# Optimization experiments

Hardware: AMD Instinct MI355X
Metric: run time of the kernel (lower is better)

## Reference

```python
import jax, jax.numpy as jnp
import numpy as np

M2 = 512  # config['sketch_dim_AV']; seq_len must be divisible by M2


def setup_inputs() -> dict:
    key = jax.random.key(0)
    kq, kk, kv = jax.random.split(key, 3)
    B, H, N, D = 4, 16, 4096, 64
    Q = jax.random.normal(kq, (B, H, N, D), dtype=jnp.float32)
    K = jax.random.normal(kk, (B, H, N, D), dtype=jnp.float32)
    V = jax.random.normal(kv, (B, H, N, D), dtype=jnp.float32)
    mask = jnp.ones((B, N), dtype=jnp.float32)  # unused: self.mask == False
    return {"Q": Q, "K": K, "V": V, "mask": mask}


def reference(Q, K, V, mask):
    # SketchingAttention.forward with sketch_QT=False, method='averaging',
    # sketch_AV=True, use_relu=False, skip_V=True, mask disabled.
    B, H, N, D = Q.shape
    scale = D ** 0.5
    # right_sketch_3D on KS = K.transpose(-1,-2) (shape b,h,d,n):
    # torch does reshape(b*h, d, n) -> reshape(b, h, m2, n//m2, d).mean(-2).
    # Row-major reshape semantics match jnp.reshape exactly, including the
    # intentional (d,n)->(m2, n//m2, d) block reinterpretation.
    SKS = jnp.swapaxes(K, -1, -2).reshape(B, H, M2, N // M2, D).mean(axis=-2)  # (B,H,M2,D)
    # compute_attn(QS, SKS): softmax(Q @ SKS^T / sqrt(d)) over the sketch axis
    logits = jnp.einsum('bhnd,bhmd->bhnm', Q, SKS) / scale  # (B,H,N,M2)
    A_est = jax.nn.softmax(logits, axis=-1)
    # ST_V: chunk-average V along the sequence into M2 buckets
    ST_V = V.reshape(B, H, M2, N // M2, D).mean(axis=-2)  # (B,H,M2,D)
    AV_est = jnp.einsum('bhnm,bhmd->bhnd', A_est, ST_V)
    return AV_est + V  # skip_V residual
```

## Files before the change

kernel.cpp:

```cpp
#include <hip/hip_runtime.h>

using short8 = __attribute__((ext_vector_type(8))) short;
using f32x4  = __attribute__((ext_vector_type(4))) float;

constexpr int NN = 4096;
constexpr int DD = 64;
constexpr int MM = 512;
constexpr int BH = 64;

__device__ __forceinline__ short f2bf(float f) {
    union { float f; unsigned u; } v; v.f = f;
    unsigned r = v.u + 0x7FFF + ((v.u >> 16) & 1);
    return (short)(r >> 16);
}

__device__ __forceinline__ unsigned cvt_pk_bf16(float lo, float hi) {
    unsigned r;
    asm("v_cvt_pk_bf16_f32 %0, %1, %2" : "=v"(r) : "v"(lo), "v"(hi));
    return r;
}

__global__ __launch_bounds__(1024) void sketch_kernel(
    const float* __restrict__ K, const float* __restrict__ V,
    short* __restrict__ sks, short* __restrict__ stvT) {
    __shared__ float lds[64][65];
    const int t  = threadIdx.x;
    const int lo = t & 63;
    const int hi = t >> 6;
    const int bh = blockIdx.x >> 3;
    const int g  = blockIdx.x & 7;
    const float* Kb = K + ((size_t)bh * NN + g * 512) * DD;
    const float* Vb = V + ((size_t)bh * NN + g * 512) * DD;

#pragma unroll
    for (int i = 0; i < 4; ++i) {
        int e = hi * 4 + i;
        float s = 0.f;
#pragma unroll
        for (int c = 0; c < 8; ++c)
            s += Kb[(size_t)(c * 64 + e) * DD + lo];
        lds[e][lo] = s * 0.125f;
    }
    __syncthreads();
#pragma unroll
    for (int i = 0; i < 4; ++i) {
        int d = hi * 4 + i;
        sks[((size_t)bh * MM + d * 8 + g) * DD + lo] = f2bf(lds[lo][d]);
    }
    __syncthreads();
#pragma unroll
    for (int i = 0; i < 4; ++i) {
        int ml = hi * 4 + i;
        float s = 0.f;
#pragma unroll
        for (int c = 0; c < 8; ++c)
            s += Vb[(size_t)(ml * 8 + c) * DD + lo];
        lds[ml][lo] = s * 0.125f;
    }
    __syncthreads();
    const int pm = ((lo & 0x1C) << 1) | ((lo & 0x20) >> 3) | (lo & 3);
#pragma unroll
    for (int i = 0; i < 4; ++i) {
        int e = hi * 4 + i;
        stvT[((size_t)bh * DD + e) * MM + g * 64 + pm] = f2bf(lds[lo][e]);
    }
}

__global__ __launch_bounds__(256, 2) void attn_kernel(
    const float* __restrict__ Q, const float* __restrict__ V,
    const short* __restrict__ sks, const short* __restrict__ stvT,
    float* __restrict__ out) {
    __shared__ __align__(16) short sks_s[2][64][72];
    __shared__ __align__(16) short stv_s[2][64][72];

    const int tid  = threadIdx.x;
    const int wave = tid >> 6;
    const int lane = tid & 63;
    const int quad = lane >> 4;
    const int l16  = lane & 15;
    const int bh   = blockIdx.x >> 4;
    const int rb   = (blockIdx.x & 15) * 256 + wave * 64;

    const short* sksb = sks + (size_t)bh * MM * DD;
    const short* stvb = stvT + (size_t)bh * DD * MM;

    short8 aq[4][2];
#pragma unroll
    for (int t = 0; t < 4; ++t) {
        const float* qr = Q + ((size_t)bh * NN + rb + t * 16 + l16) * DD;
#pragma unroll
        for (int kc = 0; kc < 2; ++kc) {
            f32x4 f0 = *(const f32x4*)&qr[kc * 32 + quad * 8];
            f32x4 f1 = *(const f32x4*)&qr[kc * 32 + quad * 8 + 4];
#pragma unroll
            for (int j = 0; j < 4; ++j) {
                aq[t][kc][j]     = f2bf(f0[j] * 0.125f);
                aq[t][kc][j + 4] = f2bf(f1[j] * 0.125f);
            }
        }
    }

    f32x4 O[4][4];
#pragma unroll
    for (int t = 0; t < 4; ++t)
#pragma unroll
        for (int nb = 0; nb < 4; ++nb) O[t][nb] = (f32x4){0.f, 0.f, 0.f, 0.f};
    float psum[4] = {0.f, 0.f, 0.f, 0.f};

    const int srow = tid >> 2;
    const int scol = (tid & 3) * 16;
    short8 pfk0, pfk1, pfv0, pfv1;

    {
        const short* gk = sksb + (size_t)srow * DD + scol;
        const short* gv = stvb + (size_t)srow * MM + scol;
        pfk0 = *(const short8*)gk;  pfk1 = *(const short8*)(gk + 8);
        pfv0 = *(const short8*)gv;  pfv1 = *(const short8*)(gv + 8);
        *(short8*)&sks_s[0][srow][scol]     = pfk0;
        *(short8*)&sks_s[0][srow][scol + 8] = pfk1;
        *(short8*)&stv_s[0][srow][scol]     = pfv0;
        *(short8*)&stv_s[0][srow][scol + 8] = pfv1;
        const short* gk1 = sksb + (size_t)64 * DD + (size_t)srow * DD + scol;
        const short* gv1 = stvb + (size_t)srow * MM + 64 + scol;
        pfk0 = *(const short8*)gk1; pfk1 = *(const short8*)(gk1 + 8);
        pfv0 = *(const short8*)gv1; pfv1 = *(const short8*)(gv1 + 8);
    }
    __syncthreads();

    for (int mc = 0; mc < 8; ++mc) {
        const int p = mc & 1;
        if (mc < 7) {
            *(short8*)&sks_s[p ^ 1][srow][scol]     = pfk0;
            *(short8*)&sks_s[p ^ 1][srow][scol + 8] = pfk1;
            *(short8*)&stv_s[p ^ 1][srow][scol]     = pfv0;
            *(short8*)&stv_s[p ^ 1][srow][scol + 8] = pfv1;
        }
        if (mc < 6) {
            const short* gk = sksb + (size_t)(mc + 2) * 64 * DD + (size_t)srow * DD + scol;
            const short* gv = stvb + (size_t)srow * MM + (mc + 2) * 64 + scol;
            pfk0 = *(const short8*)gk;  pfk1 = *(const short8*)(gk + 8);
            pfv0 = *(const short8*)gv;  pfv1 = *(const short8*)(gv + 8);
        }

        unsigned pk[4][4][2];
#pragma unroll
        for (int jb = 0; jb < 4; ++jb) {
            f32x4 s[4];
#pragma unroll
            for (int t = 0; t < 4; ++t) s[t] = (f32x4){0.f, 0.f, 0.f, 0.f};
#pragma unroll
            for (int kc = 0; kc < 2; ++kc) {
                short8 am = *(const short8*)&sks_s[p][jb * 16 + l16][kc * 32 + quad * 8];
#pragma unroll
                for (int t = 0; t < 4; ++t)
                    s[t] = __builtin_amdgcn_mfma_f32_16x16x32_bf16(am, aq[t][kc], s[t], 0, 0, 0);
            }
#pragma unroll
            for (int t = 0; t < 4; ++t)
#pragma unroll
                for (int rp = 0; rp < 2; ++rp) {
                    float e0 = __expf(s[t][2 * rp]), e1 = __expf(s[t][2 * rp + 1]);
                    psum[t] += e0 + e1;
                    pk[t][jb][rp] = cvt_pk_bf16(e0, e1);
                }
        }

        short8 ap[4][2];
#pragma unroll
        for (int t = 0; t < 4; ++t) {
            union { unsigned u[4]; short8 s; } u0, u1;
            u0.u[0] = pk[t][0][0]; u0.u[1] = pk[t][0][1];
            u0.u[2] = pk[t][2][0]; u0.u[3] = pk[t][2][1];
            u1.u[0] = pk[t][1][0]; u1.u[1] = pk[t][1][1];
            u1.u[2] = pk[t][3][0]; u1.u[3] = pk[t][3][1];
            ap[t][0] = u0.s; ap[t][1] = u1.s;
        }

#pragma unroll
        for (int kc = 0; kc < 2; ++kc)
#pragma unroll
            for (int nb = 0; nb < 4; ++nb) {
                short8 b = *(const short8*)&stv_s[p][nb * 16 + l16][kc * 32 + quad * 8];
#pragma unroll
                for (int t = 0; t < 4; ++t)
                    O[t][nb] = __builtin_amdgcn_mfma_f32_16x16x32_bf16(ap[t][kc], b, O[t][nb], 0, 0, 0);
            }

        __syncthreads();
    }

    float inv[4];
#pragma unroll
    for (int t = 0; t < 4; ++t) {
        float s = psum[t];
        s += __shfl_xor(s, 16);
        s += __shfl_xor(s, 32);
        inv[t] = 1.0f / s;
    }
#pragma unroll
    for (int t = 0; t < 4; ++t)
#pragma unroll
        for (int r = 0; r < 4; ++r) {
            float iv = __shfl(inv[t], quad * 4 + r);
#pragma unroll
            for (int nb = 0; nb < 4; ++nb) {
                size_t idx = ((size_t)bh * NN + rb + t * 16 + quad * 4 + r) * DD + nb * 16 + l16;
                out[idx] = O[t][nb][r] * iv + V[idx];
            }
        }
}

extern "C" void kernel_launch(void* const* d_in, const int* in_sizes, int n_in,
                              void* d_out, int out_size, void* d_ws, size_t ws_size,
                              hipStream_t stream) {
    const float* Q = (const float*)d_in[0];
    const float* K = (const float*)d_in[1];
    const float* V = (const float*)d_in[2];
    float* out = (float*)d_out;

    short* sks  = (short*)d_ws;
    short* stvT = sks + (size_t)BH * MM * DD;

    sketch_kernel<<<BH * 8, 1024, 0, stream>>>(K, V, sks, stvT);
    attn_kernel<<<BH * (NN / 256), 256, 0, stream>>>(Q, V, sks, stvT, out);
}
```

Measured before the change: 245.6 us.

## Stage full sketch tiles in LDS once and drop per-chunk double buffering

The attention kernel now loads the entire per-head SKS and ST_V sketches (512x64 bf16 each) into shared memory up front. The loop over sketch chunks then runs without per-iteration barriers or register prefetch. Blocks grow to 512 threads covering 512 rows, so each sketch load is shared by twice as many rows. In exchange LDS use rises to about 147 KB per block, which caps occupancy, and the global loads are no longer overlapped with compute.

New measurement: 255.4 us. 1.04x slower.

```diff
diff --git a/kernel.cpp b/kernel.cpp
--- a/kernel.cpp
+++ b/kernel.cpp
@@ -66,23 +66,35 @@
     }
 }
 
-__global__ __launch_bounds__(256, 2) void attn_kernel(
+__global__ __launch_bounds__(512, 2) void attn_kernel(
     const float* __restrict__ Q, const float* __restrict__ V,
     const short* __restrict__ sks, const short* __restrict__ stvT,
     float* __restrict__ out) {
-    __shared__ __align__(16) short sks_s[2][64][72];
-    __shared__ __align__(16) short stv_s[2][64][72];
+    __shared__ __align__(16) short sks_s[8][64][72];
+    __shared__ __align__(16) short stv_s[8][64][72];
 
     const int tid  = threadIdx.x;
     const int wave = tid >> 6;
     const int lane = tid & 63;
     const int quad = lane >> 4;
     const int l16  = lane & 15;
-    const int bh   = blockIdx.x >> 4;
-    const int rb   = (blockIdx.x & 15) * 256 + wave * 64;
+    const int bh   = blockIdx.x >> 3;
+    const int rb   = (blockIdx.x & 7) * 512 + wave * 64;
 
     const short* sksb = sks + (size_t)bh * MM * DD;
     const short* stvb = stvT + (size_t)bh * DD * MM;
+
+    {
+        const int srow = tid >> 3;
+        const int scol = (tid & 7) * 8;
+#pragma unroll
+        for (int mc = 0; mc < 8; ++mc) {
+            const short* gk = sksb + (size_t)(mc * 64 + srow) * DD + scol;
+            const short* gv = stvb + (size_t)srow * MM + mc * 64 + scol;
+            *(short8*)&sks_s[mc][srow][scol] = *(const short8*)gk;
+            *(short8*)&stv_s[mc][srow][scol] = *(const short8*)gv;
+        }
+    }
 
     short8 aq[4][2];
 #pragma unroll
@@ -107,41 +119,10 @@
         for (int nb = 0; nb < 4; ++nb) O[t][nb] = (f32x4){0.f, 0.f, 0.f, 0.f};
     float psum[4] = {0.f, 0.f, 0.f, 0.f};
 
-    const int srow = tid >> 2;
-    const int scol = (tid & 3) * 16;
-    short8 pfk0, pfk1, pfv0, pfv1;
-
-    {
-        const short* gk = sksb + (size_t)srow * DD + scol;
-        const short* gv = stvb + (size_t)srow * MM + scol;
-        pfk0 = *(const short8*)gk;  pfk1 = *(const short8*)(gk + 8);
-        pfv0 = *(const short8*)gv;  pfv1 = *(const short8*)(gv + 8);
-        *(short8*)&sks_s[0][srow][scol]     = pfk0;
-        *(short8*)&sks_s[0][srow][scol + 8] = pfk1;
-        *(short8*)&stv_s[0][srow][scol]     = pfv0;
-        *(short8*)&stv_s[0][srow][scol + 8] = pfv1;
-        const short* gk1 = sksb + (size_t)64 * DD + (size_t)srow * DD + scol;
-        const short* gv1 = stvb + (size_t)srow * MM + 64 + scol;
-        pfk0 = *(const short8*)gk1; pfk1 = *(const short8*)(gk1 + 8);
-        pfv0 = *(const short8*)gv1; pfv1 = *(const short8*)(gv1 + 8);
-    }
-    __syncthreads();
-
+    __syncthreads();
+
+#pragma unroll 2
     for (int mc = 0; mc < 8; ++mc) {
-        const int p = mc & 1;
-        if (mc < 7) {
-            *(short8*)&sks_s[p ^ 1][srow][scol]     = pfk0;
-            *(short8*)&sks_s[p ^ 1][srow][scol + 8] = pfk1;
-            *(short8*)&stv_s[p ^ 1][srow][scol]     = pfv0;
-            *(short8*)&stv_s[p ^ 1][srow][scol + 8] = pfv1;
-        }
-        if (mc < 6) {
-            const short* gk = sksb + (size_t)(mc + 2) * 64 * DD + (size_t)srow * DD + scol;
-            const short* gv = stvb + (size_t)srow * MM + (mc + 2) * 64 + scol;
-            pfk0 = *(const short8*)gk;  pfk1 = *(const short8*)(gk + 8);
-            pfv0 = *(const short8*)gv;  pfv1 = *(const short8*)(gv + 8);
-        }
-
         unsigned pk[4][4][2];
 #pragma unroll
         for (int jb = 0; jb < 4; ++jb) {
@@ -150,7 +131,7 @@
             for (int t = 0; t < 4; ++t) s[t] = (f32x4){0.f, 0.f, 0.f, 0.f};
 #pragma unroll
             for (int kc = 0; kc < 2; ++kc) {
-                short8 am = *(const short8*)&sks_s[p][jb * 16 + l16][kc * 32 + quad * 8];
+                short8 am = *(const short8*)&sks_s[mc][jb * 16 + l16][kc * 32 + quad * 8];
 #pragma unroll
                 for (int t = 0; t < 4; ++t)
                     s[t] = __builtin_amdgcn_mfma_f32_16x16x32_bf16(am, aq[t][kc], s[t], 0, 0, 0);
@@ -180,13 +161,11 @@
         for (int kc = 0; kc < 2; ++kc)
 #pragma unroll
             for (int nb = 0; nb < 4; ++nb) {
-                short8 b = *(const short8*)&stv_s[p][nb * 16 + l16][kc * 32 + quad * 8];
+                short8 b = *(const short8*)&stv_s[mc][nb * 16 + l16][kc * 32 + quad * 8];
 #pragma unroll
                 for (int t = 0; t < 4; ++t)
                     O[t][nb] = __builtin_amdgcn_mfma_f32_16x16x32_bf16(ap[t][kc], b, O[t][nb], 0, 0, 0);
             }
-
-        __syncthreads();
     }
 
     float inv[4];
@@ -222,5 +201,5 @@
     short* stvT = sks + (size_t)BH * MM * DD;
 
     sketch_kernel<<<BH * 8, 1024, 0, stream>>>(K, V, sks, stvT);
-    attn_kernel<<<BH * (NN / 256), 256, 0, stream>>>(Q, V, sks, stvT, out);
-}
+    attn_kernel<<<BH * (NN / 512), 512, 0, stream>>>(Q, V, sks, stvT, out);
+}
```
